# Kernel tuning notes

Hardware: AMD Instinct MI355X
Metric: run time of the kernel (lower is better)

## Reference

```python
import jax, jax.numpy as jnp
import numpy as np


def _gcn_conv(x, edge_index, W, b):
    # PyG GCNConv: h = D^{-1/2} (A + I) D^{-1/2} (x @ W) + b
    n = x.shape[0]
    xw = x @ W  # [N, C]
    loop = jnp.arange(n, dtype=edge_index.dtype)
    row = jnp.concatenate([edge_index[0], loop])  # source (x_j)
    col = jnp.concatenate([edge_index[1], loop])  # target (aggregation index)
    deg = jax.ops.segment_sum(jnp.ones_like(col, dtype=xw.dtype), col, num_segments=n)
    dinv = jnp.where(deg > 0, deg ** -0.5, 0.0)
    norm = dinv[row] * dinv[col]  # [E+N]
    out = jax.ops.segment_sum(xw[row] * norm[:, None], col, num_segments=n)
    return out + b


def setup_inputs() -> dict:
    key = jax.random.key(0)
    ks = jax.random.split(key, 8)
    N, F, E = 100000, 512, 3200000
    W_SCALE = 0.1  # keep sigmoid un-saturated
    x = jax.random.normal(ks[0], (N, F), dtype=jnp.float32)
    edge_index = jax.random.randint(ks[1], (2, E), 0, N, dtype=jnp.int64)
    Wg = jax.random.normal(ks[2], (F, 16), dtype=jnp.float32) * W_SCALE
    bg = jnp.zeros((16,), dtype=jnp.float32)
    W1 = jax.random.normal(ks[3], (16, 16), dtype=jnp.float32) * W_SCALE
    b1 = jnp.zeros((16,), dtype=jnp.float32)
    W2 = jax.random.normal(ks[4], (16, 32), dtype=jnp.float32) * W_SCALE
    b2 = jnp.zeros((32,), dtype=jnp.float32)
    W3 = jax.random.normal(ks[5], (32, 1), dtype=jnp.float32) * W_SCALE
    b3 = jnp.zeros((1,), dtype=jnp.float32)
    return {"x": x, "edge_index": edge_index, "Wg": Wg, "bg": bg,
            "W1": W1, "b1": b1, "W2": W2, "b2": b2, "W3": W3, "b3": b3}


def reference(x, edge_index, Wg, bg, W1, b1, W2, b2, W3, b3):
    h = jax.nn.relu(_gcn_conv(x, edge_index, Wg, bg))
    h = jax.nn.relu(h @ W1 + b1)
    h = jax.nn.relu(h @ W2 + b2)
    return jax.nn.sigmoid(h @ W3 + b3)  # [N, 1]
```

## Files before the change

### kernel.cpp

```cpp
#include <hip/hip_runtime.h>
#include <math.h>


static constexpr int F = 512;
static constexpr int C = 16;
static constexpr int BSH = 7;
static constexpr int BSZ = 128;
static constexpr int NBMAX = 1024;
static constexpr int EPB = 16384;

__global__ __launch_bounds__(256) void k_xw(const float* __restrict__ x,
                                            const float* __restrict__ Wg,
                                            float* __restrict__ xw, int n)
{
    int row = blockIdx.x * 256 + threadIdx.x;
    if (row >= n) return;
    float acc[C];
#pragma unroll
    for (int c = 0; c < C; ++c) acc[c] = 0.f;
    const float4* xr = (const float4*)(x + (size_t)row * F);
#pragma unroll 4
    for (int k4 = 0; k4 < F / 4; ++k4) {
        float4 xv = xr[k4];
        const float* w = Wg + k4 * 4 * C;
#pragma unroll
        for (int j = 0; j < 4; ++j) {
            float xs = (j == 0) ? xv.x : (j == 1) ? xv.y : (j == 2) ? xv.z : xv.w;
#pragma unroll
            for (int c = 0; c < C; ++c)
                acc[c] = fmaf(xs, w[j * C + c], acc[c]);
        }
    }
    float4* o = (float4*)(xw + (size_t)row * C);
#pragma unroll
    for (int q = 0; q < 4; ++q)
        o[q] = make_float4(acc[4 * q + 0], acc[4 * q + 1], acc[4 * q + 2], acc[4 * q + 3]);
}

__global__ __launch_bounds__(256) void k_bcount(const int* __restrict__ dst,
                                                int* __restrict__ bh, int E)
{
    __shared__ int hist[NBMAX];
    for (int i = threadIdx.x; i < NBMAX; i += 256) hist[i] = 0;
    __syncthreads();
    int base = blockIdx.x * EPB;
#pragma unroll 4
    for (int j = 0; j < EPB / 256; ++j) {
        int e = base + j * 256 + threadIdx.x;
        if (e < E) atomicAdd(&hist[dst[e] >> BSH], 1);
    }
    __syncthreads();
    int* row = bh + (size_t)blockIdx.x * NBMAX;
    for (int i = threadIdx.x; i < NBMAX; i += 256) row[i] = hist[i];
}

__global__ __launch_bounds__(256) void k_colscan(int* __restrict__ bh,
                                                 int* __restrict__ total, int geb)
{
    int b = blockIdx.x * 256 + threadIdx.x;
    int run = 0;
#pragma unroll 4
    for (int g = 0; g < geb; ++g) {
        size_t idx = (size_t)g * NBMAX + b;
        int v = bh[idx];
        bh[idx] = run;
        run += v;
    }
    total[b] = run;
}

__global__ __launch_bounds__(1024) void k_bscan(const int* __restrict__ total,
                                                int* __restrict__ bstart)
{
    __shared__ int sh[NBMAX];
    int t = threadIdx.x;
    int v = total[t];
    sh[t] = v;
    __syncthreads();
    for (int d = 1; d < NBMAX; d <<= 1) {
        int u = (t >= d) ? sh[t - d] : 0;
        __syncthreads();
        sh[t] += u;
        __syncthreads();
    }
    bstart[t] = sh[t] - v;
    if (t == NBMAX - 1) bstart[NBMAX] = sh[t];
}

__global__ __launch_bounds__(256) void k_bscatter(const int* __restrict__ ei,
                                                  const int* __restrict__ bh,
                                                  const int* __restrict__ bstart,
                                                  int* __restrict__ packed, int E)
{
    __shared__ int cur[NBMAX];
    int g = blockIdx.x;
    const int* row = bh + (size_t)g * NBMAX;
    for (int i = threadIdx.x; i < NBMAX; i += 256) cur[i] = bstart[i] + row[i];
    __syncthreads();
    int base = g * EPB;
#pragma unroll 2
    for (int j = 0; j < EPB / 256; ++j) {
        int e = base + j * 256 + threadIdx.x;
        if (e < E) {
            int d = ei[E + e];
            int s = ei[e];
            int b = d >> BSH;
            int r = atomicAdd(&cur[b], 1);
            packed[r] = s | ((d & (BSZ - 1)) << 17);
        }
    }
}

__global__ __launch_bounds__(256) void k_bcsr(const int* __restrict__ packed,
                                              const int* __restrict__ bstart,
                                              float* __restrict__ y,
                                              int* __restrict__ srcs,
                                              int* __restrict__ starts,
                                              int* __restrict__ cnt,
                                              float* __restrict__ dinv, int n)
{
    int b = blockIdx.x, t = threadIdx.x;
    __shared__ int hist[BSZ];
    __shared__ int sc[BSZ];
    __shared__ float sdi[BSZ];
    if (t < BSZ) hist[t] = 0;
    __syncthreads();
    int beg = bstart[b], end = bstart[b + 1];
    for (int e = beg + t; e < end; e += 256)
        atomicAdd(&hist[(packed[e] >> 17) & (BSZ - 1)], 1);
    __syncthreads();
    int myc = 0;
    if (t < BSZ) { myc = hist[t]; sc[t] = myc; }
    __syncthreads();
    for (int d = 1; d < BSZ; d <<= 1) {
        int u = 0;
        if (t < BSZ && t >= d) u = sc[t - d];
        __syncthreads();
        if (t < BSZ) sc[t] += u;
        __syncthreads();
    }
    int node0 = b << BSH;
    if (t < BSZ) {
        int lst = sc[t] - myc;
        sc[t] = lst;
        float di = rsqrtf((float)(myc + 1));
        sdi[t] = di;
        int node = node0 + t;
        if (node < n) { starts[node] = beg + lst; cnt[node] = myc; dinv[node] = di; }
        hist[t] = 0;
    }
    __syncthreads();
    for (int e = beg + t; e < end; e += 256) {
        int p = packed[e];
        int dl = (p >> 17) & (BSZ - 1);
        int r = atomicAdd(&hist[dl], 1);
        srcs[beg + sc[dl] + r] = p & 0x1FFFF;
    }
    int nn = n - node0; if (nn > BSZ) nn = BSZ;
    if (nn <= 0) return;
    int lim = nn * 4;
    float4* yv = (float4*)(y + (size_t)node0 * C);
    for (int i = t; i < lim; i += 256) {
        float di = sdi[i >> 2];
        float4 v = yv[i];
        v.x *= di; v.y *= di; v.z *= di; v.w *= di;
        yv[i] = v;
    }
}

__global__ __launch_bounds__(256) void k_gather(const float* __restrict__ y,
                                                const int* __restrict__ srcs,
                                                const int* __restrict__ starts,
                                                const int* __restrict__ cnt,
                                                const float* __restrict__ dinv,
                                                const float* __restrict__ bg,
                                                float* __restrict__ h, int n)
{
    int tid = blockIdx.x * 256 + threadIdx.x;
    int i = tid >> 2;
    if (i >= n) return;
    int q = tid & 3;
    const float4* yv = (const float4*)y;
    float4 acc = yv[(size_t)i * 4 + q];
    int beg = starts[i];
    int end = beg + cnt[i];
    int e = beg;
    int headEnd = (beg + 3) & ~3;
    if (headEnd > end) headEnd = end;
    for (; e < headEnd; ++e) {
        float4 v = yv[(size_t)srcs[e] * 4 + q];
        acc.x += v.x; acc.y += v.y; acc.z += v.z; acc.w += v.w;
    }
    for (; e + 4 <= end; e += 4) {
        int4 s4 = *(const int4*)(srcs + e);
        float4 v0 = yv[(size_t)s4.x * 4 + q];
        float4 v1 = yv[(size_t)s4.y * 4 + q];
        float4 v2 = yv[(size_t)s4.z * 4 + q];
        float4 v3 = yv[(size_t)s4.w * 4 + q];
        acc.x += v0.x + v1.x + v2.x + v3.x;
        acc.y += v0.y + v1.y + v2.y + v3.y;
        acc.z += v0.z + v1.z + v2.z + v3.z;
        acc.w += v0.w + v1.w + v2.w + v3.w;
    }
    for (; e < end; ++e) {
        float4 v = yv[(size_t)srcs[e] * 4 + q];
        acc.x += v.x; acc.y += v.y; acc.z += v.z; acc.w += v.w;
    }
    float di = dinv[i];
    const float* bq = bg + q * 4;
    float4 r;
    r.x = fmaxf(fmaf(acc.x, di, bq[0]), 0.f);
    r.y = fmaxf(fmaf(acc.y, di, bq[1]), 0.f);
    r.z = fmaxf(fmaf(acc.z, di, bq[2]), 0.f);
    r.w = fmaxf(fmaf(acc.w, di, bq[3]), 0.f);
    ((float4*)(h + (size_t)i * C))[q] = r;
}

__global__ __launch_bounds__(256) void k_mlp(const float* __restrict__ hbuf,
                                             const float* __restrict__ W1,
                                             const float* __restrict__ b1,
                                             const float* __restrict__ W2,
                                             const float* __restrict__ b2,
                                             const float* __restrict__ W3,
                                             const float* __restrict__ b3,
                                             float* __restrict__ out, int n)
{
    int i = blockIdx.x * 256 + threadIdx.x;
    if (i >= n) return;
    float h[16];
    const float4* hr = (const float4*)(hbuf + (size_t)i * C);
#pragma unroll
    for (int q = 0; q < 4; ++q) {
        float4 v = hr[q];
        h[4 * q + 0] = v.x; h[4 * q + 1] = v.y; h[4 * q + 2] = v.z; h[4 * q + 3] = v.w;
    }
    float h1[16];
#pragma unroll
    for (int c = 0; c < 16; ++c) {
        float s = b1[c];
#pragma unroll
        for (int k = 0; k < 16; ++k) s = fmaf(h[k], W1[k * 16 + c], s);
        h1[c] = fmaxf(s, 0.f);
    }
    float h2[32];
#pragma unroll
    for (int c = 0; c < 32; ++c) {
        float s = b2[c];
#pragma unroll
        for (int k = 0; k < 16; ++k) s = fmaf(h1[k], W2[k * 32 + c], s);
        h2[c] = fmaxf(s, 0.f);
    }
    float s = b3[0];
#pragma unroll
    for (int k = 0; k < 32; ++k) s = fmaf(h2[k], W3[k], s);
    out[i] = 1.f / (1.f + expf(-s));
}

extern "C" void kernel_launch(void* const* d_in, const int* in_sizes, int n_in,
                              void* d_out, int out_size, void* d_ws, size_t ws_size,
                              hipStream_t stream)
{
    const float* x  = (const float*)d_in[0];
    const int*   ei = (const int*)d_in[1];
    const float* Wg = (const float*)d_in[2];
    const float* bg = (const float*)d_in[3];
    const float* W1 = (const float*)d_in[4];
    const float* b1 = (const float*)d_in[5];
    const float* W2 = (const float*)d_in[6];
    const float* b2 = (const float*)d_in[7];
    const float* W3 = (const float*)d_in[8];
    const float* b3 = (const float*)d_in[9];
    float* out = (float*)d_out;

    int n = in_sizes[0] / F;
    int E = in_sizes[1] / 2;

    int gb  = (n + 255) / 256;
    int geb = (E + EPB - 1) / EPB;
    int NB  = (n + BSZ - 1) >> BSH;

    char* ws = (char*)d_ws;
    size_t off = 0;
    float* y      = (float*)(ws + off); off += (size_t)n * C * sizeof(float);
    float* h      = (float*)(ws + off); off += (size_t)n * C * sizeof(float);
    int*   packed = (int*)  (ws + off); off += (size_t)E * sizeof(int);
    int*   srcs   = (int*)  (ws + off);
    int*   bh     = srcs;
    size_t big = (size_t)E; if ((size_t)geb * NBMAX > big) big = (size_t)geb * NBMAX;
    off += big * sizeof(int);
    int*   starts = (int*)  (ws + off); off += (size_t)((n + 3) & ~3) * sizeof(int);
    int*   cnt    = (int*)  (ws + off); off += (size_t)((n + 3) & ~3) * sizeof(int);
    float* dinv   = (float*)(ws + off); off += (size_t)((n + 3) & ~3) * sizeof(float);
    int*   total  = (int*)  (ws + off); off += NBMAX * sizeof(int);
    int*   bstart = (int*)  (ws + off);

    k_xw<<<gb, 256, 0, stream>>>(x, Wg, y, n);
    k_bcount<<<geb, 256, 0, stream>>>(ei + E, bh, E);
    k_colscan<<<NBMAX / 256, 256, 0, stream>>>(bh, total, geb);
    k_bscan<<<1, 1024, 0, stream>>>(total, bstart);
    k_bscatter<<<geb, 256, 0, stream>>>(ei, bh, bstart, packed, E);
    k_bcsr<<<NB, 256, 0, stream>>>(packed, bstart, y, srcs, starts, cnt, dinv, n);
    k_gather<<<(n * 4 + 255) / 256, 256, 0, stream>>>(y, srcs, starts, cnt, dinv, bg, h, n);
    k_mlp<<<gb, 256, 0, stream>>>(h, W1, b1, W2, b2, W3, b3, out, n);
}
```

Before: 509.4 us.

## Fuse gather with MLP and transpose block histogram with smaller edge chunks

Measured after the change: 818.2 us. +60.6%, slower.

```diff
diff --git a/kernel.cpp b/kernel.cpp
--- a/kernel.cpp
+++ b/kernel.cpp
@@ -7,7 +7,7 @@
 static constexpr int BSH = 7;
 static constexpr int BSZ = 128;
 static constexpr int NBMAX = 1024;
-static constexpr int EPB = 16384;
+static constexpr int EPB = 4096;
 
 __global__ __launch_bounds__(256) void k_xw(const float* __restrict__ x,
                                             const float* __restrict__ Wg,
@@ -38,7 +38,7 @@
 }
 
 __global__ __launch_bounds__(256) void k_bcount(const int* __restrict__ dst,
-                                                int* __restrict__ bh, int E)
+                                                int* __restrict__ bh, int E, int geb)
 {
     __shared__ int hist[NBMAX];
     for (int i = threadIdx.x; i < NBMAX; i += 256) hist[i] = 0;
@@ -50,20 +50,19 @@
         if (e < E) atomicAdd(&hist[dst[e] >> BSH], 1);
     }
     __syncthreads();
-    int* row = bh + (size_t)blockIdx.x * NBMAX;
-    for (int i = threadIdx.x; i < NBMAX; i += 256) row[i] = hist[i];
+    for (int i = threadIdx.x; i < NBMAX; i += 256)
+        bh[(size_t)i * geb + blockIdx.x] = hist[i];
 }
 
 __global__ __launch_bounds__(256) void k_colscan(int* __restrict__ bh,
                                                  int* __restrict__ total, int geb)
 {
     int b = blockIdx.x * 256 + threadIdx.x;
+    int* row = bh + (size_t)b * geb;
     int run = 0;
-#pragma unroll 4
     for (int g = 0; g < geb; ++g) {
-        size_t idx = (size_t)g * NBMAX + b;
-        int v = bh[idx];
-        bh[idx] = run;
+        int v = row[g];
+        row[g] = run;
         run += v;
     }
     total[b] = run;
@@ -90,12 +89,12 @@
 __global__ __launch_bounds__(256) void k_bscatter(const int* __restrict__ ei,
                                                   const int* __restrict__ bh,
                                                   const int* __restrict__ bstart,
-                                                  int* __restrict__ packed, int E)
+                                                  int* __restrict__ packed, int E, int geb)
 {
     __shared__ int cur[NBMAX];
     int g = blockIdx.x;
-    const int* row = bh + (size_t)g * NBMAX;
-    for (int i = threadIdx.x; i < NBMAX; i += 256) cur[i] = bstart[i] + row[i];
+    for (int i = threadIdx.x; i < NBMAX; i += 256)
+        cur[i] = bstart[i] + bh[(size_t)i * geb + g];
     __syncthreads();
     int base = g * EPB;
 #pragma unroll 2
@@ -168,13 +167,19 @@
     }
 }
 
-__global__ __launch_bounds__(256) void k_gather(const float* __restrict__ y,
-                                                const int* __restrict__ srcs,
-                                                const int* __restrict__ starts,
-                                                const int* __restrict__ cnt,
-                                                const float* __restrict__ dinv,
-                                                const float* __restrict__ bg,
-                                                float* __restrict__ h, int n)
+__global__ __launch_bounds__(256) void k_gather_mlp(const float* __restrict__ y,
+                                                    const int* __restrict__ srcs,
+                                                    const int* __restrict__ starts,
+                                                    const int* __restrict__ cnt,
+                                                    const float* __restrict__ dinv,
+                                                    const float* __restrict__ bg,
+                                                    const float* __restrict__ W1,
+                                                    const float* __restrict__ b1,
+                                                    const float* __restrict__ W2,
+                                                    const float* __restrict__ b2,
+                                                    const float* __restrict__ W3,
+                                                    const float* __restrict__ b3,
+                                                    float* __restrict__ out, int n)
 {
     int tid = blockIdx.x * 256 + threadIdx.x;
     int i = tid >> 2;
@@ -208,40 +213,25 @@
     }
     float di = dinv[i];
     const float* bq = bg + q * 4;
-    float4 r;
-    r.x = fmaxf(fmaf(acc.x, di, bq[0]), 0.f);
-    r.y = fmaxf(fmaf(acc.y, di, bq[1]), 0.f);
-    r.z = fmaxf(fmaf(acc.z, di, bq[2]), 0.f);
-    r.w = fmaxf(fmaf(acc.w, di, bq[3]), 0.f);
-    ((float4*)(h + (size_t)i * C))[q] = r;
-}
-
-__global__ __launch_bounds__(256) void k_mlp(const float* __restrict__ hbuf,
-                                             const float* __restrict__ W1,
-                                             const float* __restrict__ b1,
-                                             const float* __restrict__ W2,
-                                             const float* __restrict__ b2,
-                                             const float* __restrict__ W3,
-                                             const float* __restrict__ b3,
-                                             float* __restrict__ out, int n)
-{
-    int i = blockIdx.x * 256 + threadIdx.x;
-    if (i >= n) return;
-    float h[16];
-    const float4* hr = (const float4*)(hbuf + (size_t)i * C);
-#pragma unroll
-    for (int q = 0; q < 4; ++q) {
-        float4 v = hr[q];
-        h[4 * q + 0] = v.x; h[4 * q + 1] = v.y; h[4 * q + 2] = v.z; h[4 * q + 3] = v.w;
+    float r0 = fmaxf(fmaf(acc.x, di, bq[0]), 0.f);
+    float r1 = fmaxf(fmaf(acc.y, di, bq[1]), 0.f);
+    float r2 = fmaxf(fmaf(acc.z, di, bq[2]), 0.f);
+    float r3 = fmaxf(fmaf(acc.w, di, bq[3]), 0.f);
+    const float* w1r = W1 + q * 4 * 16;
+    float p1[16];
+#pragma unroll
+    for (int c = 0; c < 16; ++c)
+        p1[c] = fmaf(r0, w1r[c],
+                fmaf(r1, w1r[16 + c],
+                fmaf(r2, w1r[32 + c], r3 * w1r[48 + c])));
+#pragma unroll
+    for (int c = 0; c < 16; ++c) {
+        p1[c] += __shfl_xor(p1[c], 1);
+        p1[c] += __shfl_xor(p1[c], 2);
     }
     float h1[16];
 #pragma unroll
-    for (int c = 0; c < 16; ++c) {
-        float s = b1[c];
-#pragma unroll
-        for (int k = 0; k < 16; ++k) s = fmaf(h[k], W1[k * 16 + c], s);
-        h1[c] = fmaxf(s, 0.f);
-    }
+    for (int c = 0; c < 16; ++c) h1[c] = fmaxf(p1[c] + b1[c], 0.f);
     float h2[32];
 #pragma unroll
     for (int c = 0; c < 32; ++c) {
@@ -253,7 +243,7 @@
     float s = b3[0];
 #pragma unroll
     for (int k = 0; k < 32; ++k) s = fmaf(h2[k], W3[k], s);
-    out[i] = 1.f / (1.f + expf(-s));
+    if (q == 0) out[i] = 1.f / (1.f + expf(-s));
 }
 
 extern "C" void kernel_launch(void* const* d_in, const int* in_sizes, int n_in,
@@ -282,11 +272,10 @@
     char* ws = (char*)d_ws;
     size_t off = 0;
     float* y      = (float*)(ws + off); off += (size_t)n * C * sizeof(float);
-    float* h      = (float*)(ws + off); off += (size_t)n * C * sizeof(float);
     int*   packed = (int*)  (ws + off); off += (size_t)E * sizeof(int);
     int*   srcs   = (int*)  (ws + off);
     int*   bh     = srcs;
-    size_t big = (size_t)E; if ((size_t)geb * NBMAX > big) big = (size_t)geb * NBMAX;
+    size_t big = (size_t)E; if ((size_t)NBMAX * geb > big) big = (size_t)NBMAX * geb;
     off += big * sizeof(int);
     int*   starts = (int*)  (ws + off); off += (size_t)((n + 3) & ~3) * sizeof(int);
     int*   cnt    = (int*)  (ws + off); off += (size_t)((n + 3) & ~3) * sizeof(int);
@@ -295,11 +284,11 @@
     int*   bstart = (int*)  (ws + off);
 
     k_xw<<<gb, 256, 0, stream>>>(x, Wg, y, n);
-    k_bcount<<<geb, 256, 0, stream>>>(ei + E, bh, E);
+    k_bcount<<<geb, 256, 0, stream>>>(ei + E, bh, E, geb);
     k_colscan<<<NBMAX / 256, 256, 0, stream>>>(bh, total, geb);
     k_bscan<<<1, 1024, 0, stream>>>(total, bstart);
-    k_bscatter<<<geb, 256, 0, stream>>>(ei, bh, bstart, packed, E);
+    k_bscatter<<<geb, 256, 0, stream>>>(ei, bh, bstart, packed, E, geb);
     k_bcsr<<<NB, 256, 0, stream>>>(packed, bstart, y, srcs, starts, cnt, dinv, n);
-    k_gather<<<(n * 4 + 255) / 256, 256, 0, stream>>>(y, srcs, starts, cnt, dinv, bg, h, n);
-    k_mlp<<<gb, 256, 0, stream>>>(h, W1, b1, W2, b2, W3, b3, out, n);
-}
+    k_gather_mlp<<<(n * 4 + 255) / 256, 256, 0, stream>>>(y, srcs, starts, cnt, dinv,
+                                                          bg, W1, b1, W2, b2, W3, b3, out, n);
+}
```
